# Kernel optimization log

Hardware: AMD Instinct MI355X
Metric: run time of the kernel (lower is better)

The kernel has to match this reference:

```python
import jax, jax.numpy as jnp
import numpy as np

B, H, W, C = 32, 112, 112, 192
KH = KW = 3


def setup_inputs() -> dict:
    key = jax.random.key(0)
    k1, k2 = jax.random.split(key)
    x = jax.random.normal(k1, (B, H, W, C), dtype=jnp.float32)
    # depthwise kernel, HWIO with I=1 and feature_group_count=C (depth_multiplier=1)
    w = jax.random.normal(k2, (KH, KW, 1, C), dtype=jnp.float32) * 0.1
    b = jnp.zeros((C,), dtype=jnp.float32)
    return {"x": x, "w": w, "b": b}


def reference(x, w, b):
    # Depthwise conv = grouped conv with feature_group_count == channels_in.
    # stride 1, 'same' padding, dilation 1, depth_multiplier 1, linear activation.
    out = jax.lax.conv_general_dilated(
        x, w,
        window_strides=(1, 1),
        padding='SAME',
        rhs_dilation=(1, 1),
        dimension_numbers=('NHWC', 'HWIO', 'NHWC'),
        feature_group_count=C,
    )
    return out + b  # bias broadcast over channel axis
```

## Files before the change

kernel.cpp:

```cpp
#include <hip/hip_runtime.h>


constexpr int Bn = 32, Hn = 112, Wn = 112, Cn = 192, C4 = 48;
constexpr int WT = 16, CT = 8;
constexpr int WTiles = 7, CTiles = 6;
constexpr int NSTEP = 14, HG = 2;
constexpr int LWC = 18;
constexpr int ROWF4 = LWC * CT;
constexpr int REGF4 = 4 * ROWF4;
constexpr int REGB = REGF4 * 16;
constexpr int NSLOT = 4;

typedef float floatx4 __attribute__((ext_vector_type(4)));

#define VMWAIT(n) asm volatile("s_waitcnt vmcnt(" #n ")" ::: "memory")

__device__ __forceinline__ floatx4 fma4(floatx4 a, floatx4 b, floatx4 c) {
  c.x = fmaf(a.x, b.x, c.x);
  c.y = fmaf(a.y, b.y, c.y);
  c.z = fmaf(a.z, b.z, c.z);
  c.w = fmaf(a.w, b.w, c.w);
  return c;
}

__global__ __launch_bounds__(128, 2) void dwconv3x3_deep(
    const float* __restrict__ x,
    const float* __restrict__ wgt,
    const float* __restrict__ bias,
    float* __restrict__ out) {
  __shared__ floatx4 lds[NSLOT * REGF4];
  const int tid = (int)threadIdx.x;
  const int lane = tid & 63;
  const int wave = tid >> 6;

  int bid = blockIdx.x;
  int chk = gridDim.x >> 3;
  int sbid = (bid & 7) * chk + (bid >> 3);
  int c4t = sbid % CTiles; int tt = sbid / CTiles;
  int wt = tt % WTiles;    tt /= WTiles;
  int hg = tt % HG;        int b = tt / HG;

  const int hbase = hg * (4 * NSTEP);
  const int w0 = wt * WT;
  const int cbase = c4t * (CT * 4);
  const float* xb = x + (long)b * Hn * Wn * Cn;
  const int rstr = Wn * Cn;

  const int cstart = wave * 5;
  const int ccount = 5 - wave;
  int rr[5], colOff[5];
#pragma unroll
  for (int j = 0; j < 5; ++j) {
    int l = (cstart + j) * 64 + lane;
    int r = l / ROWF4;
    int rem = l - r * ROWF4;
    int wi = rem >> 3, c4l = rem & 7;
    int wg = w0 + wi - 1;
    int wc = min(max(wg, 0), Wn - 1);
    rr[j] = r;
    colOff[j] = wc * Cn + cbase + c4l * 4;
  }

#pragma unroll
  for (int k = 0; k < 3; ++k) {
#pragma unroll
    for (int j = 0; j < 5; ++j) {
      if (j < ccount) {
        int h = hbase + 4 * k + rr[j] - 1;
        int hc = min(max(h, 0), Hn - 1);
        const float* src = xb + (long)hc * rstr + colOff[j];
        char* dst = (char*)lds + k * REGB + (cstart + j) * 1024;
        __builtin_amdgcn_global_load_lds(
            (const __attribute__((address_space(1))) void*)src,
            (__attribute__((address_space(3))) void*)dst, 16, 0, 0);
      }
    }
  }

  const int c4i = tid & 7;
  const int wi1 = tid >> 3;
  const int cofs = cbase + c4i * 4;
  const int wg1 = w0 + wi1;
  const float cs0 = (wg1 >= 1) ? 1.f : 0.f;
  const float cs2 = (wg1 <= Wn - 2) ? 1.f : 0.f;
  floatx4 wv[3][3];
#pragma unroll
  for (int kh = 0; kh < 3; ++kh) {
#pragma unroll
    for (int kw = 0; kw < 3; ++kw)
      wv[kh][kw] = *(const floatx4*)(wgt + (kh * 3 + kw) * Cn + cofs);
    wv[kh][0] *= cs0;
    wv[kh][2] *= cs2;
  }
  const floatx4 bv = *(const floatx4*)(bias + cofs);
  const float sTop = (hg == 0) ? 0.f : 1.f;
  const float sBot = (hg == HG - 1) ? 0.f : 1.f;

  const int ostr = Wn * C4;
  floatx4* outp = (floatx4*)out +
      ((long)b * Hn + hbase) * ostr + (long)wg1 * C4 + c4t * CT + c4i;

#pragma unroll
  for (int t = 0; t < NSTEP; ++t) {
    if (t + 3 <= NSTEP) {
      const int k = t + 3;
      char* rbase = (char*)lds + (k & 3) * REGB;
#pragma unroll
      for (int j = 0; j < 5; ++j) {
        if (j < ccount) {
          int h = hbase + 4 * k + rr[j] - 1;
          int hc = min(h, Hn - 1);
          const float* src = xb + (long)hc * rstr + colOff[j];
          __builtin_amdgcn_global_load_lds(
              (const __attribute__((address_space(1))) void*)src,
              (__attribute__((address_space(3))) void*)(rbase + (cstart + j) * 1024),
              16, 0, 0);
        }
      }
    }
    if (t == 0)       { if (wave == 0) VMWAIT(10); else VMWAIT(8); }
    else if (t == 1)  { if (wave == 0) VMWAIT(14); else VMWAIT(12); }
    else if (t <= 11) { if (wave == 0) VMWAIT(18); else VMWAIT(16); }
    else if (t == 12) { if (wave == 0) VMWAIT(13); else VMWAIT(12); }
    else              { VMWAIT(8); }
    __builtin_amdgcn_s_barrier();

    floatx4 acc[4];
#pragma unroll
    for (int o = 0; o < 4; ++o) acc[o] = bv;

#pragma unroll
    for (int r = 0; r < 6; ++r) {
      const int reg = (r < 4) ? t : t + 1;
      const int rowoff = (r < 4) ? r : r - 4;
      const floatx4* base = lds + (reg & 3) * REGF4 + rowoff * ROWF4 + tid;
      floatx4 xv0 = base[0];
      floatx4 xv1 = base[CT];
      floatx4 xv2 = base[2 * CT];
      if (t == 0 && r == 0) { xv0 *= sTop; xv1 *= sTop; xv2 *= sTop; }
      if (t == NSTEP - 1 && r == 5) { xv0 *= sBot; xv1 *= sBot; xv2 *= sBot; }
#pragma unroll
      for (int kh = 0; kh < 3; ++kh) {
        int o = r - kh;
        if (o >= 0 && o < 4) {
          acc[o] = fma4(xv0, wv[kh][0], acc[o]);
          acc[o] = fma4(xv1, wv[kh][1], acc[o]);
          acc[o] = fma4(xv2, wv[kh][2], acc[o]);
        }
      }
    }

#pragma unroll
    for (int o = 0; o < 4; ++o)
      __builtin_nontemporal_store(acc[o], outp + (long)(4 * t + o) * ostr);

    __builtin_amdgcn_s_barrier();
  }
}

extern "C" void kernel_launch(void* const* d_in, const int* in_sizes, int n_in,
                              void* d_out, int out_size, void* d_ws, size_t ws_size,
                              hipStream_t stream) {
  const float* x = (const float*)d_in[0];
  const float* w = (const float*)d_in[1];
  const float* b = (const float*)d_in[2];
  float* out = (float*)d_out;

  const int grid = Bn * HG * WTiles * CTiles;
  dwconv3x3_deep<<<grid, 128, 0, stream>>>(x, w, b, out);
}
```

Baseline: 117.3 us.

## Restructure depthwise conv tiling with row ring buffer and register-held halo columns

Changes the tile to 16 wide by 12 float4 channels with 192 threads, and splits height into 4 groups of 7 steps. A 10-row LDS ring buffer replaces the 4-slot region scheme, which removes the second barrier per step. Edge threads now load the left and right halo columns directly into registers, so LDS no longer holds the 18-column padded rows. The goals are less redundant halo traffic through LDS, less LDS per block and higher occupancy. The cost is scattered per-thread global loads for the halo and a simpler vmcnt scheme with less prefetch depth.

```diff
diff --git a/kernel.cpp b/kernel.cpp
--- a/kernel.cpp
+++ b/kernel.cpp
@@ -2,14 +2,12 @@
 
 
 constexpr int Bn = 32, Hn = 112, Wn = 112, Cn = 192, C4 = 48;
-constexpr int WT = 16, CT = 8;
-constexpr int WTiles = 7, CTiles = 6;
-constexpr int NSTEP = 14, HG = 2;
-constexpr int LWC = 18;
-constexpr int ROWF4 = LWC * CT;
-constexpr int REGF4 = 4 * ROWF4;
-constexpr int REGB = REGF4 * 16;
-constexpr int NSLOT = 4;
+constexpr int WT = 16, CT = 12;
+constexpr int WTiles = 7, CTiles = 4;
+constexpr int NSTEP = 7, HG = 4;
+constexpr int ROWF4 = WT * CT;
+constexpr int ROWB = ROWF4 * 16;
+constexpr int RING = 10;
 
 typedef float floatx4 __attribute__((ext_vector_type(4)));
 
@@ -23,12 +21,12 @@
   return c;
 }
 
-__global__ __launch_bounds__(128, 2) void dwconv3x3_deep(
+__global__ __launch_bounds__(192, 4) void dwconv3x3_lean(
     const float* __restrict__ x,
     const float* __restrict__ wgt,
     const float* __restrict__ bias,
     float* __restrict__ out) {
-  __shared__ floatx4 lds[NSLOT * REGF4];
+  __shared__ floatx4 lds[RING * ROWF4];
   const int tid = (int)threadIdx.x;
   const int lane = tid & 63;
   const int wave = tid >> 6;
@@ -36,49 +34,72 @@
   int bid = blockIdx.x;
   int chk = gridDim.x >> 3;
   int sbid = (bid & 7) * chk + (bid >> 3);
-  int c4t = sbid % CTiles; int tt = sbid / CTiles;
-  int wt = tt % WTiles;    tt /= WTiles;
-  int hg = tt % HG;        int b = tt / HG;
+  int c4t = sbid & 3;  int tt = sbid >> 2;
+  int wt = tt % WTiles; tt /= WTiles;
+  int hg = tt & 3;      int b = tt >> 2;
 
-  const int hbase = hg * (4 * NSTEP);
+  const int hbase = hg * 28;
   const int w0 = wt * WT;
   const int cbase = c4t * (CT * 4);
   const float* xb = x + (long)b * Hn * Wn * Cn;
   const int rstr = Wn * Cn;
 
-  const int cstart = wave * 5;
-  const int ccount = 5 - wave;
-  int rr[5], colOff[5];
+  int rr4[4], ck4[4], co4[4];
 #pragma unroll
-  for (int j = 0; j < 5; ++j) {
-    int l = (cstart + j) * 64 + lane;
-    int r = l / ROWF4;
-    int rem = l - r * ROWF4;
-    int wi = rem >> 3, c4l = rem & 7;
-    int wg = w0 + wi - 1;
-    int wc = min(max(wg, 0), Wn - 1);
-    rr[j] = r;
-    colOff[j] = wc * Cn + cbase + c4l * 4;
+  for (int j = 0; j < 4; ++j) {
+    int k = 4 * wave + j;
+    rr4[j] = k / 3;  ck4[j] = k % 3;
+    int rem = ck4[j] * 64 + lane;
+    int wi = rem / 12, c4l = rem % 12;
+    co4[j] = (w0 + wi) * Cn + cbase + c4l * 4;
+  }
+  int rr2[2], ck2[2], co2[2];
+#pragma unroll
+  for (int j = 0; j < 2; ++j) {
+    int k = 2 * wave + j;
+    rr2[j] = k / 3;  ck2[j] = k % 3;
+    int rem = ck2[j] * 64 + lane;
+    int wi = rem / 12, c4l = rem % 12;
+    co2[j] = (w0 + wi) * Cn + cbase + c4l * 4;
   }
 
 #pragma unroll
-  for (int k = 0; k < 3; ++k) {
+  for (int j = 0; j < 4; ++j) {
+    int h = max(hbase + rr4[j] - 1, 0);
+    const float* src = xb + (long)h * rstr + co4[j];
+    char* dst = (char*)lds + rr4[j] * ROWB + ck4[j] * 1024;
+    __builtin_amdgcn_global_load_lds(
+        (const __attribute__((address_space(1))) void*)src,
+        (__attribute__((address_space(3))) void*)dst, 16, 0, 0);
+  }
 #pragma unroll
-    for (int j = 0; j < 5; ++j) {
-      if (j < ccount) {
-        int h = hbase + 4 * k + rr[j] - 1;
-        int hc = min(max(h, 0), Hn - 1);
-        const float* src = xb + (long)hc * rstr + colOff[j];
-        char* dst = (char*)lds + k * REGB + (cstart + j) * 1024;
-        __builtin_amdgcn_global_load_lds(
-            (const __attribute__((address_space(1))) void*)src,
-            (__attribute__((address_space(3))) void*)dst, 16, 0, 0);
-      }
+  for (int j = 0; j < 2; ++j) {
+    int row = 4 + rr2[j];
+    int h = hbase + row - 1;
+    const float* src = xb + (long)h * rstr + co2[j];
+    char* dst = (char*)lds + row * ROWB + ck2[j] * 1024;
+    __builtin_amdgcn_global_load_lds(
+        (const __attribute__((address_space(1))) void*)src,
+        (__attribute__((address_space(3))) void*)dst, 16, 0, 0);
+  }
+
+  const int c4i = tid % 12;
+  const int wi1 = tid / 12;
+  const bool edgeL = (wi1 == 0), edgeR = (wi1 == 15);
+  const bool edge = edgeL || edgeR;
+
+  int hcol = edgeL ? (w0 - 1) : (w0 + WT);
+  hcol = min(max(hcol, 0), Wn - 1);
+  const float* hp = xb + (long)hcol * Cn + cbase + c4i * 4;
+  floatx4 halo[RING];
+  if (edge) {
+#pragma unroll
+    for (int r = 0; r < 6; ++r) {
+      int h = max(hbase + r - 1, 0);
+      halo[r] = *(const floatx4*)(hp + (long)h * rstr);
     }
   }
 
-  const int c4i = tid & 7;
-  const int wi1 = tid >> 3;
   const int cofs = cbase + c4i * 4;
   const int wg1 = w0 + wi1;
   const float cs0 = (wg1 >= 1) ? 1.f : 0.f;
@@ -98,32 +119,34 @@
 
   const int ostr = Wn * C4;
   floatx4* outp = (floatx4*)out +
-      ((long)b * Hn + hbase) * ostr + (long)wg1 * C4 + c4t * CT + c4i;
+      ((long)(b * Hn + hbase) * Wn + wg1) * C4 + c4t * CT + c4i;
 
 #pragma unroll
   for (int t = 0; t < NSTEP; ++t) {
-    if (t + 3 <= NSTEP) {
-      const int k = t + 3;
-      char* rbase = (char*)lds + (k & 3) * REGB;
+    if (t == 0) { VMWAIT(0); } else { VMWAIT(4); }
+    __builtin_amdgcn_s_barrier();
+
+    if (t < NSTEP - 1) {
 #pragma unroll
-      for (int j = 0; j < 5; ++j) {
-        if (j < ccount) {
-          int h = hbase + 4 * k + rr[j] - 1;
-          int hc = min(h, Hn - 1);
-          const float* src = xb + (long)hc * rstr + colOff[j];
-          __builtin_amdgcn_global_load_lds(
-              (const __attribute__((address_space(1))) void*)src,
-              (__attribute__((address_space(3))) void*)(rbase + (cstart + j) * 1024),
-              16, 0, 0);
+      for (int j = 0; j < 4; ++j) {
+        int row = 4 * t + 6 + rr4[j];
+        int slot = row % RING;
+        int h = min(hbase + row - 1, Hn - 1);
+        const float* src = xb + (long)h * rstr + co4[j];
+        char* dst = (char*)lds + slot * ROWB + ck4[j] * 1024;
+        __builtin_amdgcn_global_load_lds(
+            (const __attribute__((address_space(1))) void*)src,
+            (__attribute__((address_space(3))) void*)dst, 16, 0, 0);
+      }
+      if (edge) {
+#pragma unroll
+        for (int j = 0; j < 4; ++j) {
+          int row = 4 * t + 6 + j;
+          int h = min(hbase + row - 1, Hn - 1);
+          halo[row % RING] = *(const floatx4*)(hp + (long)h * rstr);
         }
       }
     }
-    if (t == 0)       { if (wave == 0) VMWAIT(10); else VMWAIT(8); }
-    else if (t == 1)  { if (wave == 0) VMWAIT(14); else VMWAIT(12); }
-    else if (t <= 11) { if (wave == 0) VMWAIT(18); else VMWAIT(16); }
-    else if (t == 12) { if (wave == 0) VMWAIT(13); else VMWAIT(12); }
-    else              { VMWAIT(8); }
-    __builtin_amdgcn_s_barrier();
 
     floatx4 acc[4];
 #pragma unroll
@@ -131,12 +154,13 @@
 
 #pragma unroll
     for (int r = 0; r < 6; ++r) {
-      const int reg = (r < 4) ? t : t + 1;
-      const int rowoff = (r < 4) ? r : r - 4;
-      const floatx4* base = lds + (reg & 3) * REGF4 + rowoff * ROWF4 + tid;
-      floatx4 xv0 = base[0];
-      floatx4 xv1 = base[CT];
-      floatx4 xv2 = base[2 * CT];
+      const int row = 4 * t + r;
+      const floatx4* base = lds + (row % RING) * ROWF4 + tid;
+      floatx4 xv1 = base[0];
+      floatx4 xv0 = base[edgeL ? 0 : -CT];
+      floatx4 xv2 = base[edgeR ? 0 : CT];
+      if (edgeL) xv0 = halo[row % RING];
+      if (edgeR) xv2 = halo[row % RING];
       if (t == 0 && r == 0) { xv0 *= sTop; xv1 *= sTop; xv2 *= sTop; }
       if (t == NSTEP - 1 && r == 5) { xv0 *= sBot; xv1 *= sBot; xv2 *= sBot; }
 #pragma unroll
@@ -153,8 +177,6 @@
 #pragma unroll
     for (int o = 0; o < 4; ++o)
       __builtin_nontemporal_store(acc[o], outp + (long)(4 * t + o) * ostr);
-
-    __builtin_amdgcn_s_barrier();
   }
 }
 
@@ -167,5 +189,5 @@
   float* out = (float*)d_out;
 
   const int grid = Bn * HG * WTiles * CTiles;
-  dwconv3x3_deep<<<grid, 128, 0, stream>>>(x, w, b, out);
+  dwconv3x3_lean<<<grid, 192, 0, stream>>>(x, w, b, out);
 }
```

Result: slower. 316.4 us (+169.7%).
